# Kernel tuning notes

Measured on AMD Instinct MI355X. Metric: run time of the kernel, lower is better.

Reference implementation:

```python
import jax, jax.numpy as jnp
import numpy as np

B, IH, IW = 16, 32, 32
N = IH * IW
HEADS, DIM_HEAD = 8, 64
INNER = HEADS * DIM_HEAD  # 512
INP, OUP = 512, 512
SCALE = DIM_HEAD ** -0.5


def _relative_index():
    # replicate torch.meshgrid (ij) -> coords [2, N]
    yy, xx = np.meshgrid(np.arange(IH), np.arange(IW), indexing='ij')
    coords = np.stack([yy.reshape(-1), xx.reshape(-1)])  # [2, N]
    rel = coords[:, :, None] - coords[:, None, :]        # [2, N, N]
    rel[0] += IH - 1
    rel[1] += IW - 1
    rel[0] *= 2 * IW - 1
    return jnp.asarray(rel.sum(0).reshape(-1), dtype=jnp.int32)  # [N*N]


def setup_inputs() -> dict:
    key = jax.random.key(0)
    k1, k2, k3, k4, k5 = jax.random.split(key, 5)
    x = jax.random.normal(k1, (B, N, INP), dtype=jnp.float32)
    W_qkv = jax.random.normal(k2, (INP, 3 * INNER), dtype=jnp.float32) * (INP ** -0.5)
    # table is initialized to zeros in the module; use small randn so bias path is exercised
    rel_table = jax.random.normal(k3, ((2 * IH - 1) * (2 * IW - 1), HEADS), dtype=jnp.float32) * 0.02
    W_out = jax.random.normal(k4, (INNER, OUP), dtype=jnp.float32) * (INNER ** -0.5)
    b_out = jax.random.normal(k5, (OUP,), dtype=jnp.float32) * 0.02
    return {
        'x': x,
        'W_qkv': W_qkv,
        'rel_table': rel_table,
        'W_out': W_out,
        'b_out': b_out,
        'rel_index': _relative_index(),
    }


def reference(x, W_qkv, rel_table, W_out, b_out, rel_index):
    b, n, _ = x.shape
    qkv = x @ W_qkv                                            # [b, n, 3*inner]
    q, k, v = jnp.split(qkv, 3, axis=-1)
    def to_heads(t):
        return t.reshape(b, n, HEADS, DIM_HEAD).transpose(0, 2, 1, 3)  # [b, h, n, d]
    q, k, v = to_heads(q), to_heads(k), to_heads(v)
    dots = jnp.einsum('bhnd,bhmd->bhnm', q, k) * SCALE         # [b, h, n, n]
    bias = rel_table[rel_index].reshape(n, n, HEADS).transpose(2, 0, 1)[None]  # [1, h, n, n]
    attn = jax.nn.softmax(dots + bias, axis=-1)
    out = jnp.einsum('bhnm,bhmd->bhnd', attn, v)               # [b, h, n, d]
    out = out.transpose(0, 2, 1, 3).reshape(b, n, INNER)       # [b, n, inner]
    return out @ W_out + b_out
```

## Files before the change

kernel.cpp:

```cpp
#include <hip/hip_runtime.h>
#include <math.h>

#define BATCH 16
#define NTOK 1024
#define HEADS 8
#define DHEAD 64
#define INNER 512
#define QKV_COLS 1536
#define SCALE_L2E 0.1803368801111244f
#define LOG2E 1.4426950408889634f

#if __has_builtin(__builtin_amdgcn_exp2f)
#define EXP2F(x) __builtin_amdgcn_exp2f(x)
#else
#define EXP2F(x) __expf((x) * 0.6931471805599453f)
#endif

typedef _Float16 f16x8 __attribute__((ext_vector_type(8)));
typedef _Float16 f16x4 __attribute__((ext_vector_type(4)));
typedef float f32x4 __attribute__((ext_vector_type(4)));

#define MFMA32(a, b, c) __builtin_amdgcn_mfma_f32_16x16x32_f16(a, b, c, 0, 0, 0)

__device__ __forceinline__ void glds16(const void* g, void* l) {
    __builtin_amdgcn_global_load_lds(
        (const __attribute__((address_space(1))) unsigned int*)g,
        (__attribute__((address_space(3))) unsigned int*)l, 16, 0, 0);
}

#define XV (BATCH * NTOK * INNER / 4)
#define WQ (INNER * QKV_COLS)
#define WO (INNER * INNER)

__global__ __launch_bounds__(256)
void convert_inputs(const float* __restrict__ x, const float* __restrict__ Wq,
                    const float* __restrict__ Wo, _Float16* __restrict__ x_h,
                    _Float16* __restrict__ Wq_t, _Float16* __restrict__ Wo_t) {
    int idx = blockIdx.x * 256 + threadIdx.x;
    if (idx < XV) {
        float4 v = ((const float4*)x)[idx];
        f16x4 h;
        h[0] = (_Float16)v.x; h[1] = (_Float16)v.y;
        h[2] = (_Float16)v.z; h[3] = (_Float16)v.w;
        *(f16x4*)(x_h + (size_t)idx * 4) = h;
    } else if (idx < XV + WQ) {
        int i = idx - XV;
        int n = i >> 9, k = i & 511;
        Wq_t[i] = (_Float16)Wq[k * QKV_COLS + n];
    } else if (idx < XV + WQ + WO) {
        int i = idx - XV - WQ;
        int n = i >> 9, k = i & 511;
        Wo_t[i] = (_Float16)Wo[k * INNER + n];
    }
}

template<int MODE>
__global__ __launch_bounds__(256, 4)
void gemm_f16(const _Float16* __restrict__ A, const _Float16* __restrict__ Bt,
              const float* __restrict__ bias, void* __restrict__ Cout,
              _Float16* __restrict__ vtg, int M, int N, int K) {
    __shared__ _Float16 As[128 * 64];
    __shared__ _Float16 Bs[128 * 64];

    const int t    = threadIdx.x;
    const int l    = t & 63;
    const int w    = t >> 6;
    const int wm   = w >> 1;
    const int wn   = w & 1;
    const int quad = l >> 4;
    const int lrow = l & 15;
    const size_t row0 = (size_t)blockIdx.y * 128;
    const size_t col0 = (size_t)blockIdx.x * 128;

    const int srow = t >> 3;
    const int sch  = t & 7;

    f32x4 acc[4][4] = {};

    for (int k0 = 0; k0 < K; k0 += 64) {
        __syncthreads();
#pragma unroll
        for (int p = 0; p < 4; ++p) {
            const int r  = p * 32 + srow;
            const int gc = (sch ^ (r & 7)) * 8;
            glds16(A  + (row0 + r) * K + k0 + gc, (char*)As + p * 4096 + t * 16);
            glds16(Bt + (col0 + r) * K + k0 + gc, (char*)Bs + p * 4096 + t * 16);
        }
        __syncthreads();

#pragma unroll
        for (int ks = 0; ks < 2; ++ks) {
            f16x8 af[4], bf[4];
#pragma unroll
            for (int i = 0; i < 4; ++i) {
                const int r = wm * 64 + i * 16 + lrow;
                af[i] = *(const f16x8*)(As + r * 64 + (((ks * 4 + quad) ^ (r & 7)) * 8));
            }
#pragma unroll
            for (int j = 0; j < 4; ++j) {
                const int r = wn * 64 + j * 16 + lrow;
                bf[j] = *(const f16x8*)(Bs + r * 64 + (((ks * 4 + quad) ^ (r & 7)) * 8));
            }
#pragma unroll
            for (int i = 0; i < 4; ++i)
#pragma unroll
                for (int j = 0; j < 4; ++j)
                    acc[i][j] = MFMA32(bf[j], af[i], acc[i][j]);
        }
    }

    const bool isV = (MODE == 2) && (col0 >= 2 * INNER);
#pragma unroll
    for (int i = 0; i < 4; ++i) {
        const size_t m = row0 + wm * 64 + i * 16 + lrow;
#pragma unroll
        for (int j = 0; j < 4; ++j) {
            const size_t c = col0 + wn * 64 + j * 16 + quad * 4;
            f32x4 v = acc[i][j];
            if (MODE == 0) {
                float4 bv = *(const float4*)(bias + c);
                v[0] += bv.x; v[1] += bv.y; v[2] += bv.z; v[3] += bv.w;
                *(f32x4*)((float*)Cout + m * N + c) = v;
            } else if (!isV) {
                f16x4 hv;
                hv[0] = (_Float16)v[0]; hv[1] = (_Float16)v[1];
                hv[2] = (_Float16)v[2]; hv[3] = (_Float16)v[3];
                *(f16x4*)((_Float16*)Cout + m * N + c) = hv;
            } else {
                const int cv = (int)(c - 2 * INNER);
                const int hh = cv >> 6, db = cv & 63;
                const size_t vb = (((size_t)(m >> 10) * HEADS + hh) * 64 + db) * NTOK
                                  + (m & (NTOK - 1));
#pragma unroll
                for (int reg = 0; reg < 4; ++reg)
                    vtg[vb + (size_t)reg * NTOK] = (_Float16)v[reg];
            }
        }
    }
}

__global__ __launch_bounds__(512, 4)
void attn_f16_v6(const _Float16* __restrict__ qkv, const _Float16* __restrict__ vt,
                 const float* __restrict__ rel_table, _Float16* __restrict__ out) {
    __shared__ _Float16 Ks[2][64 * 64];
    __shared__ _Float16 Vs[2][64 * 64];
    __shared__ float biasS[3969];

    const int t    = threadIdx.x;
    const int l    = t & 63;
    const int w    = t >> 6;
    const int quad = l >> 4;
    const int lrow = l & 15;
    const int h    = blockIdx.y;
    const int bb   = blockIdx.z;
    const int qr0  = blockIdx.x * 256 + w * 32;

    for (int idx = t; idx < 3969; idx += 512)
        biasS[idx] = rel_table[idx * HEADS + h] * LOG2E;

    const size_t tokbase = (size_t)bb * NTOK;

    f16x8 aq[2][2];
#pragma unroll
    for (int mt = 0; mt < 2; ++mt)
#pragma unroll
        for (int ksi = 0; ksi < 2; ++ksi)
            aq[mt][ksi] = *(const f16x8*)(qkv + (tokbase + qr0 + mt * 16 + lrow) * QKV_COLS
                                          + h * DHEAD + ksi * 32 + quad * 8);

    f32x4 O[2][4] = {};
    float l0 = 0.f, l1 = 0.f;

    const int iy = qr0 >> 5;
    const int krow_base = 8 * (lrow >> 2) + (lrow & 3);
    const int fKl = (lrow & 3) + 4 * ((lrow >> 2) & 1);

    const int kr  = t >> 3;
    const int ksl = t & 7;
    const int fKr = (kr & 3) + 4 * ((kr >> 3) & 1);
    const _Float16* kbase = qkv + tokbase * QKV_COLS + INNER + h * DHEAD;
    const _Float16* vbase = vt + ((size_t)(bb * HEADS + h) * 64) * NTOK;

    auto stage = [&](int jt, int bufi) {
        const int j0s = jt * 64;
        glds16(kbase + (size_t)(j0s + kr) * QKV_COLS + (ksl ^ fKr) * 8, (char*)Ks[bufi] + t * 16);
        glds16(vbase + (size_t)kr * NTOK + j0s + (ksl ^ (kr & 7)) * 8,  (char*)Vs[bufi] + t * 16);
    };

    stage(0, 0);

    for (int jt = 0; jt < 16; ++jt) {
        const int buf = jt & 1;
        __syncthreads();
        if (jt < 15) stage(jt + 1, buf ^ 1);

#pragma unroll
        for (int jn0 = 0; jn0 < 2; ++jn0) {
            f16x8 pb0, pb1;
#pragma unroll
            for (int s = 0; s < 2; ++s) {
                const int krow = jn0 * 32 + krow_base + 4 * s;
                f32x4 S0 = {}, S1 = {};
#pragma unroll
                for (int ksi = 0; ksi < 2; ++ksi) {
                    f16x8 bk = *(const f16x8*)(Ks[buf] + krow * 64
                                               + (((ksi * 4 + quad) ^ fKl) * 8));
                    S0 = MFMA32(bk, aq[0][ksi], S0);
                    S1 = MFMA32(bk, aq[1][ksi], S1);
                }
                const int base = (iy - (jt * 2 + jn0) + 31) * 63 + 31 + lrow
                                 - 8 * quad - 4 * s;
                {
                    float p0 = EXP2F(fmaf(S0[0], SCALE_L2E, biasS[base - 0]));
                    float p1 = EXP2F(fmaf(S0[1], SCALE_L2E, biasS[base - 1]));
                    float p2 = EXP2F(fmaf(S0[2], SCALE_L2E, biasS[base - 2]));
                    float p3 = EXP2F(fmaf(S0[3], SCALE_L2E, biasS[base - 3]));
                    l0 += (p0 + p1) + (p2 + p3);
                    pb0[s * 4 + 0] = (_Float16)p0; pb0[s * 4 + 1] = (_Float16)p1;
                    pb0[s * 4 + 2] = (_Float16)p2; pb0[s * 4 + 3] = (_Float16)p3;
                }
                {
                    const int b1 = base + 16;
                    float p0 = EXP2F(fmaf(S1[0], SCALE_L2E, biasS[b1 - 0]));
                    float p1 = EXP2F(fmaf(S1[1], SCALE_L2E, biasS[b1 - 1]));
                    float p2 = EXP2F(fmaf(S1[2], SCALE_L2E, biasS[b1 - 2]));
                    float p3 = EXP2F(fmaf(S1[3], SCALE_L2E, biasS[b1 - 3]));
                    l1 += (p0 + p1) + (p2 + p3);
                    pb1[s * 4 + 0] = (_Float16)p0; pb1[s * 4 + 1] = (_Float16)p1;
                    pb1[s * 4 + 2] = (_Float16)p2; pb1[s * 4 + 3] = (_Float16)p3;
                }
            }

#pragma unroll
            for (int dn = 0; dn < 4; ++dn) {
                const int d = dn * 16 + lrow;
                f16x8 av = *(const f16x8*)(Vs[buf] + d * 64
                              + (((jn0 * 4 + quad) ^ (d & 7)) * 8));
                O[0][dn] = MFMA32(av, pb0, O[0][dn]);
                O[1][dn] = MFMA32(av, pb1, O[1][dn]);
            }
        }
    }

#pragma unroll
    for (int mt = 0; mt < 2; ++mt) {
        float s = mt ? l1 : l0;
        s += __shfl_xor(s, 16);
        s += __shfl_xor(s, 32);
        const float inv = 1.f / s;
        const size_t orow = (tokbase + qr0 + mt * 16 + lrow) * INNER + h * DHEAD;
#pragma unroll
        for (int dn = 0; dn < 4; ++dn) {
            const f32x4 o = O[mt][dn];
            f16x4 ov;
            ov[0] = (_Float16)(o[0] * inv); ov[1] = (_Float16)(o[1] * inv);
            ov[2] = (_Float16)(o[2] * inv); ov[3] = (_Float16)(o[3] * inv);
            *(f16x4*)(out + orow + dn * 16 + quad * 4) = ov;
        }
    }
}

extern "C" void kernel_launch(void* const* d_in, const int* in_sizes, int n_in,
                              void* d_out, int out_size, void* d_ws, size_t ws_size,
                              hipStream_t stream) {
    const float* x         = (const float*)d_in[0];
    const float* W_qkv     = (const float*)d_in[1];
    const float* rel_table = (const float*)d_in[2];
    const float* W_out     = (const float*)d_in[3];
    const float* b_out     = (const float*)d_in[4];

    _Float16* x_h   = (_Float16*)d_ws;
    _Float16* Wq_t  = x_h + (size_t)BATCH * NTOK * INNER;
    _Float16* Wo_t  = Wq_t + (size_t)INNER * QKV_COLS;
    _Float16* qkv_h = Wo_t + (size_t)INNER * INNER;
    _Float16* att_h = qkv_h + (size_t)BATCH * NTOK * QKV_COLS;
    _Float16* vt_g  = att_h + (size_t)BATCH * NTOK * INNER;

    const int M = BATCH * NTOK;

    convert_inputs<<<(XV + WQ + WO + 255) / 256, 256, 0, stream>>>(
        x, W_qkv, W_out, x_h, Wq_t, Wo_t);

    gemm_f16<2><<<dim3(QKV_COLS / 128, M / 128), 256, 0, stream>>>(
        x_h, Wq_t, nullptr, qkv_h, vt_g, M, QKV_COLS, INNER);

    attn_f16_v6<<<dim3(NTOK / 256, HEADS, BATCH), 512, 0, stream>>>(
        qkv_h, vt_g, rel_table, att_h);

    gemm_f16<0><<<dim3(INNER / 128, M / 128), 256, 0, stream>>>(
        att_h, Wo_t, b_out, d_out, nullptr, M, INNER, INNER);
}
```

Baseline: 214.2 us.

## Double-buffer GEMM LDS tiles with K-step 32 and remap blocks across XCDs

The f16 GEMM now splits its shared-memory tiles into two 128x32 buffers. It prefetches the next K slice into the idle buffer while computing on the current one, which leaves one barrier per step instead of two. The swizzle is adjusted for the 32-wide rows. Block IDs are also remapped so consecutive tiles land on the same XCD, aiming for better L2 reuse. The risks are that the smaller K step doubles loop iterations and barriers per unit of work, and that reading the current buffer may not wait for its async LDS loads to finish, depending on how glds16 handles waits.

Measured after the change: 206.8 us. -3.5%, faster.

```diff
diff --git a/kernel.cpp b/kernel.cpp
--- a/kernel.cpp
+++ b/kernel.cpp
@@ -59,8 +59,8 @@
 void gemm_f16(const _Float16* __restrict__ A, const _Float16* __restrict__ Bt,
               const float* __restrict__ bias, void* __restrict__ Cout,
               _Float16* __restrict__ vtg, int M, int N, int K) {
-    __shared__ _Float16 As[128 * 64];
-    __shared__ _Float16 Bs[128 * 64];
+    __shared__ _Float16 As[2][128 * 32];
+    __shared__ _Float16 Bs[2][128 * 32];
 
     const int t    = threadIdx.x;
     const int l    = t & 63;
@@ -69,44 +69,54 @@
     const int wn   = w & 1;
     const int quad = l >> 4;
     const int lrow = l & 15;
-    const size_t row0 = (size_t)blockIdx.y * 128;
-    const size_t col0 = (size_t)blockIdx.x * 128;
-
-    const int srow = t >> 3;
-    const int sch  = t & 7;
+
+    const int nwg = gridDim.x * gridDim.y;
+    int bid = blockIdx.x + gridDim.x * blockIdx.y;
+    bid = (bid & 7) * (nwg >> 3) + (bid >> 3);
+    const size_t row0 = (size_t)(bid / gridDim.x) * 128;
+    const size_t col0 = (size_t)(bid % gridDim.x) * 128;
+
+    const int srow = t >> 2;
+    const int sch  = t & 3;
 
     f32x4 acc[4][4] = {};
 
-    for (int k0 = 0; k0 < K; k0 += 64) {
+    const int NSTEP = K >> 5;
+
+    auto stage = [&](int kk, int bufi) {
+        const int k0 = kk * 32;
+#pragma unroll
+        for (int p = 0; p < 2; ++p) {
+            const int r  = p * 64 + srow;
+            const int gc = (sch ^ (r & 3)) * 8;
+            glds16(A  + (row0 + r) * K + k0 + gc, (char*)As[bufi] + p * 4096 + t * 16);
+            glds16(Bt + (col0 + r) * K + k0 + gc, (char*)Bs[bufi] + p * 4096 + t * 16);
+        }
+    };
+
+    stage(0, 0);
+
+    for (int kk = 0; kk < NSTEP; ++kk) {
+        const int buf = kk & 1;
         __syncthreads();
-#pragma unroll
-        for (int p = 0; p < 4; ++p) {
-            const int r  = p * 32 + srow;
-            const int gc = (sch ^ (r & 7)) * 8;
-            glds16(A  + (row0 + r) * K + k0 + gc, (char*)As + p * 4096 + t * 16);
-            glds16(Bt + (col0 + r) * K + k0 + gc, (char*)Bs + p * 4096 + t * 16);
-        }
-        __syncthreads();
-
-#pragma unroll
-        for (int ks = 0; ks < 2; ++ks) {
-            f16x8 af[4], bf[4];
-#pragma unroll
-            for (int i = 0; i < 4; ++i) {
-                const int r = wm * 64 + i * 16 + lrow;
-                af[i] = *(const f16x8*)(As + r * 64 + (((ks * 4 + quad) ^ (r & 7)) * 8));
-            }
-#pragma unroll
-            for (int j = 0; j < 4; ++j) {
-                const int r = wn * 64 + j * 16 + lrow;
-                bf[j] = *(const f16x8*)(Bs + r * 64 + (((ks * 4 + quad) ^ (r & 7)) * 8));
-            }
-#pragma unroll
-            for (int i = 0; i < 4; ++i)
-#pragma unroll
-                for (int j = 0; j < 4; ++j)
-                    acc[i][j] = MFMA32(bf[j], af[i], acc[i][j]);
-        }
+        if (kk + 1 < NSTEP) stage(kk + 1, buf ^ 1);
+
+        f16x8 af[4], bf[4];
+#pragma unroll
+        for (int i = 0; i < 4; ++i) {
+            const int r = wm * 64 + i * 16 + lrow;
+            af[i] = *(const f16x8*)(As[buf] + r * 32 + ((quad ^ (r & 3)) * 8));
+        }
+#pragma unroll
+        for (int j = 0; j < 4; ++j) {
+            const int r = wn * 64 + j * 16 + lrow;
+            bf[j] = *(const f16x8*)(Bs[buf] + r * 32 + ((quad ^ (r & 3)) * 8));
+        }
+#pragma unroll
+        for (int i = 0; i < 4; ++i)
+#pragma unroll
+            for (int j = 0; j < 4; ++j)
+                acc[i][j] = MFMA32(bf[j], af[i], acc[i][j]);
     }
 
     const bool isV = (MODE == 2) && (col0 >= 2 * INNER);
```
